# Kernel optimization log

Hardware: AMD Instinct MI355X
Metric: run time of the kernel (lower is better)

Reference implementation:

```python
import jax, jax.numpy as jnp
import numpy as np

N = 50000       # nodes
E = 800000      # edges (avg degree 16)
IN_DIM = 128
H_DIM = 96      # conv='SKP' -> h_dim unchanged
OUT_DIM = 64
NUM_LAYERS = 4
HEADS = 2       # conv='SKP' -> num_heads forced to 2


def setup_inputs() -> dict:
    key = jax.random.key(0)
    ks = jax.random.split(key, 9)
    x = jax.random.normal(ks[0], (N, IN_DIM), jnp.float32)
    edge_index = jax.random.randint(ks[1], (2, E), 0, N, dtype=jnp.int32)
    enc_w = jax.random.normal(ks[2], (IN_DIM, H_DIM), jnp.float32) / np.sqrt(IN_DIM)
    enc_b = jnp.zeros((H_DIM,), jnp.float32)
    dec_w = jax.random.normal(ks[3], (H_DIM, OUT_DIM), jnp.float32) / np.sqrt(H_DIM)
    dec_b = jnp.zeros((OUT_DIM,), jnp.float32)
    # per-layer, per-head linear transforms of the SKP conv
    conv_W = jax.random.normal(ks[4], (NUM_LAYERS, HEADS, H_DIM, H_DIM), jnp.float32) / np.sqrt(H_DIM)
    # per-layer, per-head learnable edge weights (SKP takes num_edges at init)
    conv_ew = jax.random.normal(ks[5], (NUM_LAYERS, HEADS, E), jnp.float32) * 0.1
    return {"x": x, "edge_index": edge_index, "enc_w": enc_w, "enc_b": enc_b,
            "dec_w": dec_w, "dec_b": dec_b, "conv_W": conv_W, "conv_ew": conv_ew}


def _skp_conv(h, src, dst, W, ew):
    # h: [N, d], W: [H, d, d], ew: [H, E]
    # X' = sum_h S_h X W_h  (S_h = learned edge-weighted sparse propagation)
    m = jnp.einsum('nd,hde->hne', h, W)          # [H, N, d] per-head transform
    g = m[:, src, :]                              # [H, E, d] gather at source nodes
    comb = jnp.einsum('he,hed->ed', ew, g)        # weight per edge, sum heads -> [E, d]
    return jax.ops.segment_sum(comb, dst, num_segments=N)  # scatter-add to dest


def reference(x, edge_index, enc_w, enc_b, dec_w, dec_b, conv_W, conv_ew):
    src, dst = edge_index[0], edge_index[1]
    h = jax.nn.relu(x @ enc_w + enc_b)
    for l in range(NUM_LAYERS):
        h = _skp_conv(h, src, dst, conv_W[l], conv_ew[l])
        h = jax.nn.relu(h)   # act=True
    return (h @ dec_w + dec_b, h)
```

## Files before the change

kernel.cpp:

```cpp
#include <hip/hip_runtime.h>

constexpr int IND = 128;
constexpr int HD  = 96;
constexpr int OD  = 64;
constexpr int NL  = 4;

struct F3 { float x, y, z; };

__global__ __launch_bounds__(256) void k_hist(const int* __restrict__ dst, int* __restrict__ deg, int E) {
    int e = blockIdx.x * 256 + threadIdx.x;
    if (e < E) atomicAdd(&deg[dst[e]], 1);
}

__global__ __launch_bounds__(256) void k_scan1(const int* __restrict__ deg, int* __restrict__ bsum, int n) {
    int tid = threadIdx.x;
    int base = blockIdx.x * 1024 + tid * 4;
    int s = 0;
    #pragma unroll
    for (int q = 0; q < 4; ++q) { int i = base + q; if (i < n) s += deg[i]; }
    #pragma unroll
    for (int o = 32; o > 0; o >>= 1) s += __shfl_xor(s, o);
    __shared__ int wsum[4];
    int lane = tid & 63, wid = tid >> 6;
    if (lane == 0) wsum[wid] = s;
    __syncthreads();
    if (tid == 0) bsum[blockIdx.x] = wsum[0] + wsum[1] + wsum[2] + wsum[3];
}

__global__ void k_scan2(const int* __restrict__ bsum, int* __restrict__ boff, int nb,
                        int* __restrict__ row_ptr, int n, int E) {
    int l = threadIdx.x;
    int v = (l < nb) ? bsum[l] : 0;
    int incl = v;
    #pragma unroll
    for (int o = 1; o < 64; o <<= 1) { int t = __shfl_up(incl, o); if (l >= o) incl += t; }
    if (l < nb) boff[l] = incl - v;
    if (l == 0) row_ptr[n] = E;
}

__global__ __launch_bounds__(256) void k_scan3(const int* __restrict__ deg, const int* __restrict__ boff,
                                               int* __restrict__ row_ptr, int n) {
    int tid = threadIdx.x;
    int base = blockIdx.x * 1024 + tid * 4;
    int d[4];
    #pragma unroll
    for (int q = 0; q < 4; ++q) { int i = base + q; d[q] = (i < n) ? deg[i] : 0; }
    int tsum = d[0] + d[1] + d[2] + d[3];
    int incl = tsum;
    #pragma unroll
    for (int o = 1; o < 64; o <<= 1) { int t = __shfl_up(incl, o); if ((tid & 63) >= o) incl += t; }
    __shared__ int wsum[4];
    int lane = tid & 63, wid = tid >> 6;
    if (lane == 63) wsum[wid] = incl;
    __syncthreads();
    int woff = 0;
    for (int w = 0; w < wid; ++w) woff += wsum[w];
    int run = boff[blockIdx.x] + woff + (incl - tsum);
    #pragma unroll
    for (int q = 0; q < 4; ++q) {
        int i = base + q;
        if (i < n) { row_ptr[i] = run; run += d[q]; }
    }
}

__global__ __launch_bounds__(256) void k_fill(const int* __restrict__ src, const int* __restrict__ dst,
                                              const int* __restrict__ row_ptr, int* __restrict__ cursor,
                                              int* __restrict__ srcp, int* __restrict__ eidp, int E) {
    int e = blockIdx.x * 256 + threadIdx.x;
    if (e >= E) return;
    int d = dst[e];
    int pos = atomicAdd(&cursor[d], 1);
    int slot = row_ptr[d] + pos;
    srcp[slot] = src[e];
    eidp[slot] = e;
}

__global__ __launch_bounds__(256) void k_agg(const float* __restrict__ h, const int* __restrict__ row_ptr,
                                             const int* __restrict__ srcp, const int* __restrict__ eidp,
                                             const float* __restrict__ ew0, const float* __restrict__ ew1,
                                             float* __restrict__ A0, float* __restrict__ A1, int n) {
    int g = blockIdx.x * 8 + (threadIdx.x >> 5);
    int lane = threadIdx.x & 31;
    if (g >= n) return;
    int beg = row_ptr[g], end = row_ptr[g + 1];
    float a0x = 0.f, a0y = 0.f, a0z = 0.f;
    float a1x = 0.f, a1y = 0.f, a1z = 0.f;
    int off = lane * 3;
    for (int i = beg; i < end; ++i) {
        int s = srcp[i];
        int e = eidp[i];
        float w0 = ew0[e];
        float w1 = ew1[e];
        F3 v = *(const F3*)(h + (size_t)s * HD + off);
        a0x = fmaf(w0, v.x, a0x); a0y = fmaf(w0, v.y, a0y); a0z = fmaf(w0, v.z, a0z);
        a1x = fmaf(w1, v.x, a1x); a1y = fmaf(w1, v.y, a1y); a1z = fmaf(w1, v.z, a1z);
    }
    float* p0 = A0 + (size_t)g * HD + off;
    p0[0] = a0x; p0[1] = a0y; p0[2] = a0z;
    float* p1 = A1 + (size_t)g * HD + off;
    p1[0] = a1x; p1[1] = a1y; p1[2] = a1z;
}

template<int K, int NO, bool DUAL, bool RELU, bool BIAS>
__global__ __launch_bounds__(512) void k_gemm(const float* __restrict__ A0p, const float* __restrict__ A1p,
                                              const float* __restrict__ W0p, const float* __restrict__ W1p,
                                              const float* __restrict__ bias,
                                              float* __restrict__ out, int nrows) {
    constexpr int BR = 128, KB = 32;
    constexpr int NC = NO / 32;
    __shared__ float sA[KB][BR];
    __shared__ float sW[KB][NO];
    int tid = threadIdx.x;
    int tx = tid & 31;
    int ty = tid >> 5;
    int brow = blockIdx.x * BR;

    float acc[8][NC];
    #pragma unroll
    for (int r = 0; r < 8; ++r)
        #pragma unroll
        for (int j = 0; j < NC; ++j) acc[r][j] = 0.f;

    int srow = tid >> 2;
    int squart = tid & 3;

    #pragma unroll
    for (int head = 0; head < (DUAL ? 2 : 1); ++head) {
        const float* A = (head == 0) ? A0p : A1p;
        const float* W = (head == 0) ? W0p : W1p;
        for (int kc = 0; kc < K; kc += KB) {
            __syncthreads();
            {
                int gr = brow + srow;
                const float* ap = A + (size_t)gr * K + kc;
                #pragma unroll
                for (int i = 0; i < 2; ++i) {
                    int f4 = squart + 4 * i;
                    float4 v = make_float4(0.f, 0.f, 0.f, 0.f);
                    if (gr < nrows) v = *(const float4*)(ap + 4 * f4);
                    int kk = 4 * f4;
                    sA[kk + 0][srow] = v.x;
                    sA[kk + 1][srow] = v.y;
                    sA[kk + 2][srow] = v.z;
                    sA[kk + 3][srow] = v.w;
                }
            }
            {
                const float4* wp4 = (const float4*)(W + kc * NO);
                float4* sw4 = (float4*)&sW[0][0];
                constexpr int TOT4 = KB * NO / 4;
                for (int i = tid; i < TOT4; i += 512) sw4[i] = wp4[i];
            }
            __syncthreads();
            #pragma unroll
            for (int kk = 0; kk < KB; ++kk) {
                float a[8];
                #pragma unroll
                for (int q = 0; q < 2; ++q) {
                    float4 v = *(const float4*)&sA[kk][8 * ty + 4 * q];
                    a[4 * q + 0] = v.x; a[4 * q + 1] = v.y;
                    a[4 * q + 2] = v.z; a[4 * q + 3] = v.w;
                }
                float wv[NC];
                #pragma unroll
                for (int j = 0; j < NC; ++j) wv[j] = sW[kk][tx + 32 * j];
                #pragma unroll
                for (int r = 0; r < 8; ++r)
                    #pragma unroll
                    for (int j = 0; j < NC; ++j)
                        acc[r][j] = fmaf(a[r], wv[j], acc[r][j]);
            }
        }
    }
    #pragma unroll
    for (int r = 0; r < 8; ++r) {
        int gr = brow + 8 * ty + r;
        if (gr < nrows) {
            #pragma unroll
            for (int j = 0; j < NC; ++j) {
                int c = tx + 32 * j;
                float v = acc[r][j];
                if (BIAS) v += bias[c];
                if (RELU) v = fmaxf(v, 0.f);
                out[(size_t)gr * NO + c] = v;
            }
        }
    }
}

extern "C" void kernel_launch(void* const* d_in, const int* in_sizes, int n_in,
                              void* d_out, int out_size, void* d_ws, size_t ws_size,
                              hipStream_t stream) {
    const float* x     = (const float*)d_in[0];
    const int*   ei    = (const int*)  d_in[1];
    const float* enc_w = (const float*)d_in[2];
    const float* enc_b = (const float*)d_in[3];
    const float* dec_w = (const float*)d_in[4];
    const float* dec_b = (const float*)d_in[5];
    const float* convW = (const float*)d_in[6];
    const float* convE = (const float*)d_in[7];

    const int N = in_sizes[0] / IND;
    const int E = in_sizes[1] / 2;
    const int* src = ei;
    const int* dst = ei + E;
    float* fout = (float*)d_out;

    char* wp = (char*)d_ws;
    auto carve = [&](size_t bytes) -> void* {
        void* p = (void*)wp;
        wp += (bytes + 255) & ~(size_t)255;
        return p;
    };
    int* deg     = (int*)carve(2 * (size_t)N * 4);
    int* cursor  = deg + N;
    int* row_ptr = (int*)carve(((size_t)N + 1) * 4);
    int* bsum    = (int*)carve(64 * 4);
    int* boff    = (int*)carve(64 * 4);
    int* srcp    = (int*)carve((size_t)E * 4);
    int* eidp    = (int*)carve((size_t)E * 4);
    float* hbuf  = (float*)carve((size_t)N * HD * 4);
    float* Ag0   = (float*)carve((size_t)N * HD * 4);
    float* Ag1   = (float*)carve((size_t)N * HD * 4);

    hipMemsetAsync(deg, 0, 2 * (size_t)N * 4, stream);

    int ebl = (E + 255) / 256;
    int nb  = (N + 1023) / 1024;
    k_hist<<<ebl, 256, 0, stream>>>(dst, deg, E);
    k_scan1<<<nb, 256, 0, stream>>>(deg, bsum, N);
    k_scan2<<<1, 64, 0, stream>>>(bsum, boff, nb, row_ptr, N, E);
    k_scan3<<<nb, 256, 0, stream>>>(deg, boff, row_ptr, N);
    k_fill<<<ebl, 256, 0, stream>>>(src, dst, row_ptr, cursor, srcp, eidp, E);

    int gbl = (N + 127) / 128;
    k_gemm<IND, HD, false, true, true><<<gbl, 512, 0, stream>>>(x, nullptr, enc_w, nullptr, enc_b, hbuf, N);

    float* hfin = fout + (size_t)N * OD;
    for (int l = 0; l < NL; ++l) {
        const float* W0 = convW + ((size_t)l * 2 + 0) * HD * HD;
        const float* W1 = convW + ((size_t)l * 2 + 1) * HD * HD;
        const float* e0 = convE + ((size_t)l * 2 + 0) * E;
        const float* e1 = convE + ((size_t)l * 2 + 1) * E;
        k_agg<<<(N + 7) / 8, 256, 0, stream>>>(hbuf, row_ptr, srcp, eidp, e0, e1, Ag0, Ag1, N);
        float* ho = (l == NL - 1) ? hfin : hbuf;
        k_gemm<HD, HD, true, true, false><<<gbl, 512, 0, stream>>>(Ag0, Ag1, W0, W1, nullptr, ho, N);
    }
    k_gemm<HD, OD, false, false, true><<<gbl, 512, 0, stream>>>(hfin, nullptr, dec_w, nullptr, dec_b, fout, N);
}
```

Baseline: 732.5 us.

## Pack CSR src/eid pairs, pre-permute edge weights, unroll aggregation, restructure GEMM tiling

The CSR fill now writes packed int2 (src, edge id) pairs. A new per-layer k_perm kernel gathers both heads' edge weights into CSR order as float2, so the aggregation reads them contiguously instead of through an indirection. The aggregation loop is unrolled by 4 so several row gathers are in flight at once. The GEMM is rewritten to stage whole 64-row A tiles in shared memory and read weights straight from global memory with 256 threads, and the buffers are ping-ponged so the output region serves as scratch for the permuted weights. This adds an extra permutation pass per layer and drops shared-memory staging of W.

```diff
diff --git a/kernel.cpp b/kernel.cpp
--- a/kernel.cpp
+++ b/kernel.cpp
@@ -65,19 +65,26 @@
 
 __global__ __launch_bounds__(256) void k_fill(const int* __restrict__ src, const int* __restrict__ dst,
                                               const int* __restrict__ row_ptr, int* __restrict__ cursor,
-                                              int* __restrict__ srcp, int* __restrict__ eidp, int E) {
+                                              int2* __restrict__ sep, int E) {
     int e = blockIdx.x * 256 + threadIdx.x;
     if (e >= E) return;
     int d = dst[e];
     int pos = atomicAdd(&cursor[d], 1);
-    int slot = row_ptr[d] + pos;
-    srcp[slot] = src[e];
-    eidp[slot] = e;
+    sep[row_ptr[d] + pos] = make_int2(src[e], e);
+}
+
+__global__ __launch_bounds__(256) void k_perm(const int2* __restrict__ sep,
+                                              const float* __restrict__ c0,
+                                              const float* __restrict__ c1,
+                                              float2* __restrict__ ewq, int E) {
+    int i = blockIdx.x * 256 + threadIdx.x;
+    if (i >= E) return;
+    int e = sep[i].y;
+    ewq[i] = make_float2(c0[e], c1[e]);
 }
 
 __global__ __launch_bounds__(256) void k_agg(const float* __restrict__ h, const int* __restrict__ row_ptr,
-                                             const int* __restrict__ srcp, const int* __restrict__ eidp,
-                                             const float* __restrict__ ew0, const float* __restrict__ ew1,
+                                             const int2* __restrict__ sep, const float2* __restrict__ ewq,
                                              float* __restrict__ A0, float* __restrict__ A1, int n) {
     int g = blockIdx.x * 8 + (threadIdx.x >> 5);
     int lane = threadIdx.x & 31;
@@ -86,14 +93,29 @@
     float a0x = 0.f, a0y = 0.f, a0z = 0.f;
     float a1x = 0.f, a1y = 0.f, a1z = 0.f;
     int off = lane * 3;
-    for (int i = beg; i < end; ++i) {
-        int s = srcp[i];
-        int e = eidp[i];
-        float w0 = ew0[e];
-        float w1 = ew1[e];
-        F3 v = *(const F3*)(h + (size_t)s * HD + off);
-        a0x = fmaf(w0, v.x, a0x); a0y = fmaf(w0, v.y, a0y); a0z = fmaf(w0, v.z, a0z);
-        a1x = fmaf(w1, v.x, a1x); a1y = fmaf(w1, v.y, a1y); a1z = fmaf(w1, v.z, a1z);
+    int i = beg;
+    for (; i + 4 <= end; i += 4) {
+        int2 s0 = sep[i], s1 = sep[i + 1], s2 = sep[i + 2], s3 = sep[i + 3];
+        float2 w0 = ewq[i], w1 = ewq[i + 1], w2 = ewq[i + 2], w3 = ewq[i + 3];
+        F3 v0 = *(const F3*)(h + (size_t)s0.x * HD + off);
+        F3 v1 = *(const F3*)(h + (size_t)s1.x * HD + off);
+        F3 v2 = *(const F3*)(h + (size_t)s2.x * HD + off);
+        F3 v3 = *(const F3*)(h + (size_t)s3.x * HD + off);
+        a0x = fmaf(w0.x, v0.x, a0x); a0y = fmaf(w0.x, v0.y, a0y); a0z = fmaf(w0.x, v0.z, a0z);
+        a1x = fmaf(w0.y, v0.x, a1x); a1y = fmaf(w0.y, v0.y, a1y); a1z = fmaf(w0.y, v0.z, a1z);
+        a0x = fmaf(w1.x, v1.x, a0x); a0y = fmaf(w1.x, v1.y, a0y); a0z = fmaf(w1.x, v1.z, a0z);
+        a1x = fmaf(w1.y, v1.x, a1x); a1y = fmaf(w1.y, v1.y, a1y); a1z = fmaf(w1.y, v1.z, a1z);
+        a0x = fmaf(w2.x, v2.x, a0x); a0y = fmaf(w2.x, v2.y, a0y); a0z = fmaf(w2.x, v2.z, a0z);
+        a1x = fmaf(w2.y, v2.x, a1x); a1y = fmaf(w2.y, v2.y, a1y); a1z = fmaf(w2.y, v2.z, a1z);
+        a0x = fmaf(w3.x, v3.x, a0x); a0y = fmaf(w3.x, v3.y, a0y); a0z = fmaf(w3.x, v3.z, a0z);
+        a1x = fmaf(w3.y, v3.x, a1x); a1y = fmaf(w3.y, v3.y, a1y); a1z = fmaf(w3.y, v3.z, a1z);
+    }
+    for (; i < end; ++i) {
+        int2 s0 = sep[i];
+        float2 w0 = ewq[i];
+        F3 v0 = *(const F3*)(h + (size_t)s0.x * HD + off);
+        a0x = fmaf(w0.x, v0.x, a0x); a0y = fmaf(w0.x, v0.y, a0y); a0z = fmaf(w0.x, v0.z, a0z);
+        a1x = fmaf(w0.y, v0.x, a1x); a1y = fmaf(w0.y, v0.y, a1y); a1z = fmaf(w0.y, v0.z, a1z);
     }
     float* p0 = A0 + (size_t)g * HD + off;
     p0[0] = a0x; p0[1] = a0y; p0[2] = a0z;
@@ -102,87 +124,75 @@
 }
 
 template<int K, int NO, bool DUAL, bool RELU, bool BIAS>
-__global__ __launch_bounds__(512) void k_gemm(const float* __restrict__ A0p, const float* __restrict__ A1p,
-                                              const float* __restrict__ W0p, const float* __restrict__ W1p,
+__global__ __launch_bounds__(256) void k_gemm(const float* __restrict__ A0p, const float* __restrict__ A1p,
+                                              const float* __restrict__ W0p,
                                               const float* __restrict__ bias,
-                                              float* __restrict__ out, int nrows) {
-    constexpr int BR = 128, KB = 32;
+                                              float* __restrict__ out, int n) {
     constexpr int NC = NO / 32;
-    __shared__ float sA[KB][BR];
-    __shared__ float sW[KB][NO];
+    constexpr int F4 = K / 4;
+    __shared__ float sA0[64][K];
+    __shared__ float sA1[DUAL ? 64 : 1][DUAL ? K : 1];
     int tid = threadIdx.x;
+    int brow = blockIdx.x * 64;
+
+    for (int j = tid; j < 64 * F4; j += 256) {
+        int r = j / F4, c4 = j % F4;
+        int gr = brow + r;
+        float4 v = make_float4(0.f, 0.f, 0.f, 0.f);
+        if (gr < n) v = *(const float4*)(A0p + (size_t)gr * K + 4 * c4);
+        *(float4*)&sA0[r][4 * c4] = v;
+        if (DUAL) {
+            float4 u = make_float4(0.f, 0.f, 0.f, 0.f);
+            if (gr < n) u = *(const float4*)(A1p + (size_t)gr * K + 4 * c4);
+            *(float4*)&sA1[r][4 * c4] = u;
+        }
+    }
+    __syncthreads();
+
     int tx = tid & 31;
     int ty = tid >> 5;
-    int brow = blockIdx.x * BR;
-
     float acc[8][NC];
     #pragma unroll
     for (int r = 0; r < 8; ++r)
         #pragma unroll
         for (int j = 0; j < NC; ++j) acc[r][j] = 0.f;
 
-    int srow = tid >> 2;
-    int squart = tid & 3;
-
     #pragma unroll
     for (int head = 0; head < (DUAL ? 2 : 1); ++head) {
-        const float* A = (head == 0) ? A0p : A1p;
-        const float* W = (head == 0) ? W0p : W1p;
-        for (int kc = 0; kc < K; kc += KB) {
-            __syncthreads();
-            {
-                int gr = brow + srow;
-                const float* ap = A + (size_t)gr * K + kc;
+        const float* Wh = W0p + (size_t)head * K * NO;
+        #pragma unroll 1
+        for (int kb = 0; kb < K; kb += 4) {
+            float4 a4[8];
+            #pragma unroll
+            for (int r = 0; r < 8; ++r)
+                a4[r] = head ? *(const float4*)&sA1[8 * ty + r][kb]
+                             : *(const float4*)&sA0[8 * ty + r][kb];
+            #pragma unroll
+            for (int q = 0; q < 4; ++q) {
+                float wv[NC];
                 #pragma unroll
-                for (int i = 0; i < 2; ++i) {
-                    int f4 = squart + 4 * i;
-                    float4 v = make_float4(0.f, 0.f, 0.f, 0.f);
-                    if (gr < nrows) v = *(const float4*)(ap + 4 * f4);
-                    int kk = 4 * f4;
-                    sA[kk + 0][srow] = v.x;
-                    sA[kk + 1][srow] = v.y;
-                    sA[kk + 2][srow] = v.z;
-                    sA[kk + 3][srow] = v.w;
+                for (int j = 0; j < NC; ++j) wv[j] = Wh[(size_t)(kb + q) * NO + NC * tx + j];
+                #pragma unroll
+                for (int r = 0; r < 8; ++r) {
+                    const float* ap = (const float*)&a4[r];
+                    float av = ap[q];
+                    #pragma unroll
+                    for (int j = 0; j < NC; ++j) acc[r][j] = fmaf(av, wv[j], acc[r][j]);
                 }
             }
-            {
-                const float4* wp4 = (const float4*)(W + kc * NO);
-                float4* sw4 = (float4*)&sW[0][0];
-                constexpr int TOT4 = KB * NO / 4;
-                for (int i = tid; i < TOT4; i += 512) sw4[i] = wp4[i];
-            }
-            __syncthreads();
-            #pragma unroll
-            for (int kk = 0; kk < KB; ++kk) {
-                float a[8];
-                #pragma unroll
-                for (int q = 0; q < 2; ++q) {
-                    float4 v = *(const float4*)&sA[kk][8 * ty + 4 * q];
-                    a[4 * q + 0] = v.x; a[4 * q + 1] = v.y;
-                    a[4 * q + 2] = v.z; a[4 * q + 3] = v.w;
-                }
-                float wv[NC];
-                #pragma unroll
-                for (int j = 0; j < NC; ++j) wv[j] = sW[kk][tx + 32 * j];
-                #pragma unroll
-                for (int r = 0; r < 8; ++r)
-                    #pragma unroll
-                    for (int j = 0; j < NC; ++j)
-                        acc[r][j] = fmaf(a[r], wv[j], acc[r][j]);
-            }
         }
     }
     #pragma unroll
     for (int r = 0; r < 8; ++r) {
         int gr = brow + 8 * ty + r;
-        if (gr < nrows) {
+        if (gr < n) {
+            float* op = out + (size_t)gr * NO + NC * tx;
             #pragma unroll
             for (int j = 0; j < NC; ++j) {
-                int c = tx + 32 * j;
                 float v = acc[r][j];
-                if (BIAS) v += bias[c];
+                if (BIAS) v += bias[NC * tx + j];
                 if (RELU) v = fmaxf(v, 0.f);
-                out[(size_t)gr * NO + c] = v;
+                op[j] = v;
             }
         }
     }
@@ -212,16 +222,17 @@
         wp += (bytes + 255) & ~(size_t)255;
         return p;
     };
-    int* deg     = (int*)carve(2 * (size_t)N * 4);
-    int* cursor  = deg + N;
-    int* row_ptr = (int*)carve(((size_t)N + 1) * 4);
-    int* bsum    = (int*)carve(64 * 4);
-    int* boff    = (int*)carve(64 * 4);
-    int* srcp    = (int*)carve((size_t)E * 4);
-    int* eidp    = (int*)carve((size_t)E * 4);
-    float* hbuf  = (float*)carve((size_t)N * HD * 4);
-    float* Ag0   = (float*)carve((size_t)N * HD * 4);
-    float* Ag1   = (float*)carve((size_t)N * HD * 4);
+    int*    deg     = (int*)carve(2 * (size_t)N * 4);
+    int*    cursor  = deg + N;
+    int*    row_ptr = (int*)carve(((size_t)N + 1) * 4);
+    int*    bsum    = (int*)carve(64 * 4);
+    int*    boff    = (int*)carve(64 * 4);
+    int2*   sep     = (int2*)carve((size_t)E * 8);
+    float*  P0      = (float*)carve((size_t)N * HD * 4);
+    float*  P1      = (float*)carve((size_t)N * HD * 4);
+    float*  P2      = (float*)carve((size_t)N * HD * 4);
+
+    float2* ewq = (float2*)fout;
 
     hipMemsetAsync(deg, 0, 2 * (size_t)N * 4, stream);
 
@@ -231,20 +242,24 @@
     k_scan1<<<nb, 256, 0, stream>>>(deg, bsum, N);
     k_scan2<<<1, 64, 0, stream>>>(bsum, boff, nb, row_ptr, N, E);
     k_scan3<<<nb, 256, 0, stream>>>(deg, boff, row_ptr, N);
-    k_fill<<<ebl, 256, 0, stream>>>(src, dst, row_ptr, cursor, srcp, eidp, E);
-
-    int gbl = (N + 127) / 128;
-    k_gemm<IND, HD, false, true, true><<<gbl, 512, 0, stream>>>(x, nullptr, enc_w, nullptr, enc_b, hbuf, N);
-
+    k_fill<<<ebl, 256, 0, stream>>>(src, dst, row_ptr, cursor, sep, E);
+
+    int gbl64 = (N + 63) / 64;
+    int gbl8  = (N + 7) / 8;
     float* hfin = fout + (size_t)N * OD;
+
+    k_gemm<IND, HD, false, true, true><<<gbl64, 256, 0, stream>>>(x, nullptr, enc_w, enc_b, P0, N);
+
+    float* hin[NL]  = { P0, P1, P0, P1 };
+    float* ha0[NL]  = { P1, P0, P1, P0 };
+    float* hout[NL] = { P1, P0, P1, hfin };
     for (int l = 0; l < NL; ++l) {
-        const float* W0 = convW + ((size_t)l * 2 + 0) * HD * HD;
-        const float* W1 = convW + ((size_t)l * 2 + 1) * HD * HD;
-        const float* e0 = convE + ((size_t)l * 2 + 0) * E;
-        const float* e1 = convE + ((size_t)l * 2 + 1) * E;
-        k_agg<<<(N + 7) / 8, 256, 0, stream>>>(hbuf, row_ptr, srcp, eidp, e0, e1, Ag0, Ag1, N);
-        float* ho = (l == NL - 1) ? hfin : hbuf;
-        k_gemm<HD, HD, true, true, false><<<gbl, 512, 0, stream>>>(Ag0, Ag1, W0, W1, nullptr, ho, N);
-    }
-    k_gemm<HD, OD, false, false, true><<<gbl, 512, 0, stream>>>(hfin, nullptr, dec_w, nullptr, dec_b, fout, N);
-}
+        const float* c0 = convE + (size_t)(2 * l)     * E;
+        const float* c1 = convE + (size_t)(2 * l + 1) * E;
+        const float* Wl = convW + (size_t)l * 2 * HD * HD;
+        k_perm<<<ebl, 256, 0, stream>>>(sep, c0, c1, ewq, E);
+        k_agg<<<gbl8, 256, 0, stream>>>(hin[l], row_ptr, sep, ewq, ha0[l], P2, N);
+        k_gemm<HD, HD, true, true, false><<<gbl64, 256, 0, stream>>>(ha0[l], P2, Wl, nullptr, hout[l], N);
+    }
+    k_gemm<HD, OD, false, false, true><<<gbl64, 256, 0, stream>>>(hfin, nullptr, dec_w, dec_b, fout, N);
+}
```

Measured after the change: 686.4 us. 1.07x faster.
